# Kernel optimization log

Hardware: AMD Instinct MI355X
Metric: run time of the kernel (lower is better)

## Reference

```python
import jax, jax.numpy as jnp
import numpy as np

N_WORDS = 64
N_CONT_LABELS = 64
N_DISC_LABELS = 32


def _tuple_indices(n):
    # Enumerate (i, k, l, j) with i <= k, l >= k + 2, l <= j < n, matching the
    # nested Python loops in the original forward. Count is static given n.
    ii, kk, ll, jj = np.indices((n, n, n, n), dtype=np.int16)
    mask = (kk >= ii) & (ll >= kk + 2) & (jj >= ll)
    i = ii[mask].astype(np.int32)
    k = kk[mask].astype(np.int32)
    l = ll[mask].astype(np.int32)
    j = jj[mask].astype(np.int32)
    cont_idx = i * n + j                  # row of flattened disc table
    disc_idx = (k + 1) * n + (l - 1)      # row of flattened gap table
    return cont_idx, disc_idx


def setup_inputs() -> dict:
    key = jax.random.key(0)
    n, Lc, Ld = N_WORDS, N_CONT_LABELS, N_DISC_LABELS
    k0, k1, k2, k3, k4 = jax.random.split(key, 5)
    cont_weights = jax.random.normal(k0, (n, n, Lc), dtype=jnp.float32)
    disc_weights = jax.random.normal(k1, (n, n, Ld), dtype=jnp.float32)
    gap_weights = jax.random.normal(k2, (n, n, Ld), dtype=jnp.float32)
    cont_idx_np, disc_idx_np = _tuple_indices(n)  # T = 677040 for n=64
    T = cont_idx_np.shape[0]
    cont_gold = jax.random.randint(k3, (n, n), 0, Lc + 1, dtype=jnp.int32)
    disc_gold = jax.random.randint(k4, (T,), 0, Ld + 1, dtype=jnp.int32)
    return {
        "cont_weights": cont_weights,
        "disc_weights": disc_weights,
        "gap_weights": gap_weights,
        "cont_gold": cont_gold,
        "disc_gold": disc_gold,
        "cont_idx": jnp.asarray(cont_idx_np),
        "disc_idx": jnp.asarray(disc_idx_np),
    }


def reference(cont_weights, disc_weights, gap_weights, cont_gold, disc_gold,
              cont_idx, disc_idx):
    n = cont_weights.shape[0]
    Lc = cont_weights.shape[2]
    Ld = disc_weights.shape[2]
    dt = cont_weights.dtype
    null = jnp.zeros((n, n, 1), dtype=dt)

    # Continuous constituents: per-cell cross-entropy, masked to upper triangle.
    cw = jnp.concatenate([cont_weights, null], axis=-1)          # [n, n, Lc+1]
    log_z = jax.nn.logsumexp(cw, axis=-1)                        # [n, n]
    gold = jnp.take_along_axis(cw, cont_gold[..., None].astype(jnp.int32),
                               axis=-1)[..., 0]                  # [n, n]
    triu = jnp.triu(jnp.ones((n, n), dtype=dt))
    cont_loss = jnp.sum((log_z - gold) * triu)

    # Discontinuous constituents: gather rows of the two tables, add, CE-sum.
    dw = jnp.concatenate([disc_weights, null], axis=-1).reshape(-1, Ld + 1)
    gw = jnp.concatenate([gap_weights, null], axis=-1).reshape(-1, Ld + 1)
    w = dw[cont_idx] + gw[disc_idx]                              # [T, Ld+1]
    gold_d = jnp.take_along_axis(w, disc_gold[:, None].astype(jnp.int32),
                                 axis=1)[:, 0]                   # [T]
    disc_loss = jnp.sum(jax.nn.logsumexp(w, axis=-1) - gold_d)

    return cont_loss + disc_loss
```

## Files before the change

### kernel.cpp

```cpp
#include <hip/hip_runtime.h>

#define N 64
#define LC 64
#define LD 32
#define NCONT (N * N)
#define CONT_BLOCKS 16
#define NPAIRS 1953
#define RAWPAD 33

typedef __attribute__((ext_vector_type(8))) short short8;
typedef __attribute__((ext_vector_type(4))) float f32x4;

__device__ inline unsigned short f2bf(float f) {
    unsigned u = __float_as_uint(f);
    u += 0x7FFF + ((u >> 16) & 1);
    return (unsigned short)(u >> 16);
}

__device__ inline float block_sum(float v, float* ws) {
    #pragma unroll
    for (int off = 32; off > 0; off >>= 1)
        v += __shfl_down(v, off, 64);
    const int lane = threadIdx.x & 63;
    const int wid  = threadIdx.x >> 6;
    if (lane == 0) ws[wid] = v;
    __syncthreads();
    return ws[0] + ws[1] + ws[2] + ws[3];
}

__global__ __launch_bounds__(256, 4) void loss_kernel(
    const float* __restrict__ cont_w,
    const float* __restrict__ disc_w,
    const float* __restrict__ gap_w,
    const int*   __restrict__ cont_gold,
    const int*   __restrict__ disc_gold,
    float* __restrict__ partials, int T)
{
    __shared__ unsigned short EgB[64 * 32];
    __shared__ unsigned short EdB[64 * 32];
    __shared__ float Draw[62 * RAWPAD];
    __shared__ float Graw[62 * RAWPAD];
    __shared__ float ws[4];

    float acc = 0.0f;

    if (blockIdx.x < CONT_BLOCKS) {
        const int idx = blockIdx.x * 256 + threadIdx.x;
        const int i = idx >> 6, j = idx & 63;
        if (i <= j) {
            const float4* p = reinterpret_cast<const float4*>(cont_w + idx * LC);
            const int g = cont_gold[idx];
            const float goldv = (g < LC) ? cont_w[idx * LC + g] : 0.0f;
            float s0 = 1.0f, s1 = 0.0f, s2 = 0.0f, s3 = 0.0f;
            #pragma unroll
            for (int q = 0; q < LC / 4; ++q) {
                float4 x = p[q];
                s0 += __expf(x.x); s1 += __expf(x.y);
                s2 += __expf(x.z); s3 += __expf(x.w);
            }
            acc = __logf((s0 + s1) + (s2 + s3)) - goldv;
        }
    } else {
        const int w = blockIdx.x - CONT_BLOCKS;
        int k = (int)((sqrtf(8.0f * (float)w + 1.0f) - 1.0f) * 0.5f);
        while (k * (k + 1) / 2 > w) --k;
        while ((k + 1) * (k + 2) / 2 <= w) ++k;
        const int i = w - k * (k + 1) / 2;
        const int M = 62 - k;

        const float4* srcD = reinterpret_cast<const float4*>(
            disc_w + ((i << 6) + (k + 2)) * LD);
        const float4* srcG = reinterpret_cast<const float4*>(
            gap_w + (((k + 1) << 6) + (k + 1)) * LD);
        for (int e = threadIdx.x; e < 64 * 8; e += 256) {
            const int r = e >> 3, ch = e & 7;
            unsigned short* pd = &EdB[r * 32 + ch * 4];
            unsigned short* pg = &EgB[r * 32 + ch * 4];
            if (r < M) {
                float4 x = srcD[e];
                float4 y = srcG[e];
                pd[0] = f2bf(__expf(x.x)); pd[1] = f2bf(__expf(x.y));
                pd[2] = f2bf(__expf(x.z)); pd[3] = f2bf(__expf(x.w));
                pg[0] = f2bf(__expf(y.x)); pg[1] = f2bf(__expf(y.y));
                pg[2] = f2bf(__expf(y.z)); pg[3] = f2bf(__expf(y.w));
                *reinterpret_cast<float4*>(&Draw[r * RAWPAD + ch * 4]) = x;
                *reinterpret_cast<float4*>(&Graw[r * RAWPAD + ch * 4]) = y;
            } else {
                pd[0] = 0; pd[1] = 0; pd[2] = 0; pd[3] = 0;
                pg[0] = 0; pg[1] = 0; pg[2] = 0; pg[3] = 0;
            }
        }
        __syncthreads();

        const int MT = (M + 15) >> 4;
        const int ntiles = MT * (MT + 1) / 2;
        const int wid  = threadIdx.x >> 6;
        const int lane = threadIdx.x & 63;
        const int r16  = lane & 15;
        const int g4   = lane >> 4;
        for (int p = wid; p < ntiles; p += 4) {
            int tr = 0, base = 0;
            while (base + (MT - tr) <= p) { base += MT - tr; ++tr; }
            const int tc = tr + (p - base);
            short8 a = *reinterpret_cast<const short8*>(
                &EgB[(tr * 16 + r16) * 32 + g4 * 8]);
            short8 b = *reinterpret_cast<const short8*>(
                &EdB[(tc * 16 + r16) * 32 + g4 * 8]);
            f32x4 c = {0.0f, 0.0f, 0.0f, 0.0f};
            c = __builtin_amdgcn_mfma_f32_16x16x32_bf16(a, b, c, 0, 0, 0);
            #pragma unroll
            for (int q = 0; q < 4; ++q) {
                const int l = tr * 16 + g4 * 4 + q;
                const int j = tc * 16 + r16;
                if (j < M && l <= j)
                    acc += __logf(c[q] + 1.0f);
            }
        }

        const int A  = 62 - i;
        const int fA = A * (A + 1) * (A + 2) * (A + 3) / 24;
        const int hA = A * (A + 1) * (A + 2) / 6;
        const int hK = M * (M + 1) * (M + 2) / 6;
        const int t0 = (677040 - fA) + (hA - hK);
        const int cells = M * (M + 1) / 2;

        const int Bc = (cells + 255) >> 8;
        const int c0 = threadIdx.x * Bc;
        const int c1 = min(c0 + Bc, cells);
        if (c0 < c1) {
            const float twoM1 = (float)(2 * M + 1);
            int l = (int)((twoM1 - sqrtf(twoM1 * twoM1 - 8.0f * (float)c0)) * 0.5f);
            if (l < 0) l = 0; if (l > M - 1) l = M - 1;
            while (l * M - l * (l - 1) / 2 > c0) --l;
            while ((l + 1) * M - (l + 1) * l / 2 <= c0) ++l;
            int j = l + (c0 - (l * M - l * (l - 1) / 2));
            for (int c = c0; c < c1; ++c) {
                const int g = disc_gold[t0 + c];
                if (g < LD)
                    acc -= Draw[j * RAWPAD + g] + Graw[l * RAWPAD + g];
                ++j;
                if (j >= M) { ++l; j = l; }
            }
        }
    }

    const float bsum = block_sum(acc, ws);
    if (threadIdx.x == 0)
        partials[blockIdx.x] = bsum;
}

__global__ __launch_bounds__(1024) void reduce_kernel(
    const float* __restrict__ partials, float* __restrict__ out, int nblocks)
{
    float acc = 0.0f;
    for (int i = threadIdx.x; i < nblocks; i += 1024)
        acc += partials[i];
    #pragma unroll
    for (int off = 32; off > 0; off >>= 1)
        acc += __shfl_down(acc, off, 64);

    __shared__ float ws[16];
    const int lane = threadIdx.x & 63;
    const int wid  = threadIdx.x >> 6;
    if (lane == 0) ws[wid] = acc;
    __syncthreads();
    if (threadIdx.x == 0) {
        float s = 0.0f;
        #pragma unroll
        for (int w = 0; w < 16; ++w) s += ws[w];
        out[0] = s;
    }
}

extern "C" void kernel_launch(void* const* d_in, const int* in_sizes, int n_in,
                              void* d_out, int out_size, void* d_ws, size_t ws_size,
                              hipStream_t stream) {
    const float* cont_w    = (const float*)d_in[0];
    const float* disc_w    = (const float*)d_in[1];
    const float* gap_w     = (const float*)d_in[2];
    const int*   cont_gold = (const int*)d_in[3];
    const int*   disc_gold = (const int*)d_in[4];
    float* out      = (float*)d_out;
    float* partials = (float*)d_ws;
    const int T = in_sizes[4];

    const int blocks = CONT_BLOCKS + NPAIRS;
    loss_kernel<<<blocks, 256, 0, stream>>>(cont_w, disc_w, gap_w, cont_gold,
                                            disc_gold, partials, T);
    reduce_kernel<<<1, 1024, 0, stream>>>(partials, out, blocks);
}
```

Before: 13.35 us.

## Drop raw LDS tables, prefetch gold labels, and derive gold logits from bf16 exps

Removes the fp32 Draw/Graw shared-memory copies of the raw logits and recovers the gold term as log(exp(d)*exp(g)) from the bf16 exponential tables already staged for MFMA. Gold labels are now loaded with a coalesced strided pattern into registers before staging, overlapping that global latency with the table build. Staging uses packed 64-bit LDS stores and only fills MT*16 rows. It cuts LDS footprint and traffic, which may allow more blocks per CU, at the cost of a per-cell sqrt index decode and extra bf16 precision loss in the gold term.

```diff
diff --git a/kernel.cpp b/kernel.cpp
--- a/kernel.cpp
+++ b/kernel.cpp
@@ -6,15 +6,17 @@
 #define NCONT (N * N)
 #define CONT_BLOCKS 16
 #define NPAIRS 1953
-#define RAWPAD 33
 
 typedef __attribute__((ext_vector_type(8))) short short8;
 typedef __attribute__((ext_vector_type(4))) float f32x4;
 
-__device__ inline unsigned short f2bf(float f) {
+__device__ inline unsigned f2bf(float f) {
     unsigned u = __float_as_uint(f);
     u += 0x7FFF + ((u >> 16) & 1);
-    return (unsigned short)(u >> 16);
+    return u >> 16;
+}
+__device__ inline float bf2f(unsigned u) {
+    return __uint_as_float(u << 16);
 }
 
 __device__ inline float block_sum(float v, float* ws) {
@@ -38,8 +40,6 @@
 {
     __shared__ unsigned short EgB[64 * 32];
     __shared__ unsigned short EdB[64 * 32];
-    __shared__ float Draw[62 * RAWPAD];
-    __shared__ float Graw[62 * RAWPAD];
     __shared__ float ws[4];
 
     float acc = 0.0f;
@@ -68,31 +68,47 @@
         const int i = w - k * (k + 1) / 2;
         const int M = 62 - k;
 
+        const int A  = 62 - i;
+        const int fA = A * (A + 1) * (A + 2) * (A + 3) / 24;
+        const int hA = A * (A + 1) * (A + 2) / 6;
+        const int hK = M * (M + 1) * (M + 2) / 6;
+        const int t0 = (677040 - fA) + (hA - hK);
+        const int cells = M * (M + 1) / 2;
+
+        int gold_r[8];
+        #pragma unroll
+        for (int it = 0; it < 8; ++it) {
+            const int c = (int)threadIdx.x + (it << 8);
+            gold_r[it] = (c < cells) ? disc_gold[t0 + c] : LD;
+        }
+
+        const int MT   = (M + 15) >> 4;
+        const int MT16 = MT << 4;
         const float4* srcD = reinterpret_cast<const float4*>(
             disc_w + ((i << 6) + (k + 2)) * LD);
         const float4* srcG = reinterpret_cast<const float4*>(
             gap_w + (((k + 1) << 6) + (k + 1)) * LD);
-        for (int e = threadIdx.x; e < 64 * 8; e += 256) {
+        for (int e = threadIdx.x; e < MT16 * 8; e += 256) {
             const int r = e >> 3, ch = e & 7;
-            unsigned short* pd = &EdB[r * 32 + ch * 4];
-            unsigned short* pg = &EgB[r * 32 + ch * 4];
+            uint2* pd = reinterpret_cast<uint2*>(&EdB[r * 32 + ch * 4]);
+            uint2* pg = reinterpret_cast<uint2*>(&EgB[r * 32 + ch * 4]);
             if (r < M) {
                 float4 x = srcD[e];
                 float4 y = srcG[e];
-                pd[0] = f2bf(__expf(x.x)); pd[1] = f2bf(__expf(x.y));
-                pd[2] = f2bf(__expf(x.z)); pd[3] = f2bf(__expf(x.w));
-                pg[0] = f2bf(__expf(y.x)); pg[1] = f2bf(__expf(y.y));
-                pg[2] = f2bf(__expf(y.z)); pg[3] = f2bf(__expf(y.w));
-                *reinterpret_cast<float4*>(&Draw[r * RAWPAD + ch * 4]) = x;
-                *reinterpret_cast<float4*>(&Graw[r * RAWPAD + ch * 4]) = y;
+                uint2 xd = { (f2bf(__expf(x.y)) << 16) | f2bf(__expf(x.x)),
+                             (f2bf(__expf(x.w)) << 16) | f2bf(__expf(x.z)) };
+                uint2 yg = { (f2bf(__expf(y.y)) << 16) | f2bf(__expf(y.x)),
+                             (f2bf(__expf(y.w)) << 16) | f2bf(__expf(y.z)) };
+                *pd = xd;
+                *pg = yg;
             } else {
-                pd[0] = 0; pd[1] = 0; pd[2] = 0; pd[3] = 0;
-                pg[0] = 0; pg[1] = 0; pg[2] = 0; pg[3] = 0;
+                uint2 z = {0u, 0u};
+                *pd = z;
+                *pg = z;
             }
         }
         __syncthreads();
 
-        const int MT = (M + 15) >> 4;
         const int ntiles = MT * (MT + 1) / 2;
         const int wid  = threadIdx.x >> 6;
         const int lane = threadIdx.x & 63;
@@ -117,29 +133,24 @@
             }
         }
 
-        const int A  = 62 - i;
-        const int fA = A * (A + 1) * (A + 2) * (A + 3) / 24;
-        const int hA = A * (A + 1) * (A + 2) / 6;
-        const int hK = M * (M + 1) * (M + 2) / 6;
-        const int t0 = (677040 - fA) + (hA - hK);
-        const int cells = M * (M + 1) / 2;
-
-        const int Bc = (cells + 255) >> 8;
-        const int c0 = threadIdx.x * Bc;
-        const int c1 = min(c0 + Bc, cells);
-        if (c0 < c1) {
-            const float twoM1 = (float)(2 * M + 1);
-            int l = (int)((twoM1 - sqrtf(twoM1 * twoM1 - 8.0f * (float)c0)) * 0.5f);
-            if (l < 0) l = 0; if (l > M - 1) l = M - 1;
-            while (l * M - l * (l - 1) / 2 > c0) --l;
-            while ((l + 1) * M - (l + 1) * l / 2 <= c0) ++l;
-            int j = l + (c0 - (l * M - l * (l - 1) / 2));
-            for (int c = c0; c < c1; ++c) {
-                const int g = disc_gold[t0 + c];
-                if (g < LD)
-                    acc -= Draw[j * RAWPAD + g] + Graw[l * RAWPAD + g];
-                ++j;
-                if (j >= M) { ++l; j = l; }
+        const float twoM1 = (float)(2 * M + 1);
+        #pragma unroll
+        for (int it = 0; it < 8; ++it) {
+            const int c = (int)threadIdx.x + (it << 8);
+            if (c < cells) {
+                const int g = gold_r[it];
+                if (g < LD) {
+                    int l = (int)((twoM1 -
+                        sqrtf(twoM1 * twoM1 - 8.0f * (float)c)) * 0.5f);
+                    if (l < 0) l = 0;
+                    if (l > M - 1) l = M - 1;
+                    while (l * M - l * (l - 1) / 2 > c) --l;
+                    while ((l + 1) * M - (l + 1) * l / 2 <= c) ++l;
+                    const int j = l + (c - (l * M - l * (l - 1) / 2));
+                    const float ed = bf2f(EdB[j * 32 + g]);
+                    const float eg = bf2f(EgB[l * 32 + g]);
+                    acc -= __logf(ed * eg);
+                }
             }
         }
     }
```

New measurement: 13.97 us. +4.7%, slower.
